# Optimization experiments

Measured on AMD Instinct MI355X. Metric: run time of the kernel, lower is better.

## Reference

```python
import jax, jax.numpy as jnp
import numpy as np

B, TX, TS = 64, 2048, 10
D, L, NMELS, MAXR, R = 256, 1024, 80, 20, 2


def gru_cell(x, h, wih, whh, bih, bhh):
    # torch GRUCell: gates ordered (r, z, n)
    gi = x @ wih.T + bih
    gh = h @ whh.T + bhh
    ir, iz, inn = jnp.split(gi, 3, axis=-1)
    hr, hz, hn = jnp.split(gh, 3, axis=-1)
    r = jax.nn.sigmoid(ir + hr)
    z = jax.nn.sigmoid(iz + hz)
    n = jnp.tanh(inn + r * hn)
    return (1.0 - z) * n + z * h


def lstm_cell(x, h, c, wih, whh, bih, bhh):
    # torch LSTMCell: gates ordered (i, f, g, o)
    g = x @ wih.T + bih + h @ whh.T + bhh
    i, f, gg, o = jnp.split(g, 4, axis=-1)
    c_new = jax.nn.sigmoid(f) * c + jax.nn.sigmoid(i) * jnp.tanh(gg)
    h_new = jax.nn.sigmoid(o) * jnp.tanh(c_new)
    return h_new, c_new


def attention(enc, query, W, v):
    # u = v @ tanh(enc + W q); softmax over time
    qp = query @ W.T                                  # [B, D]
    u = jnp.tanh(enc + qp[:, None, :]) @ v            # [B, T]
    scores = jax.nn.softmax(u, axis=-1)               # [B, T]
    ctx = jnp.einsum('bt,btd->bd', scores, enc)       # [B, D]
    return scores, ctx


def setup_inputs() -> dict:
    key = jax.random.key(0)
    ks = jax.random.split(key, 40)
    n = lambda i, shape, s=0.02: jax.random.normal(ks[i], shape, dtype=jnp.float32) * s
    return {
        'encoder_seq': n(0, (B, TX, D), 1.0),
        'style_embed': n(1, (B, TS, D), 1.0),
        'prenet_in': n(2, (B, NMELS), 1.0),
        'h_text': n(3, (B, D), 1.0), 'h_style': n(4, (B, D), 1.0), 'h_attn': n(5, (B, D), 1.0),
        'h_r1': n(6, (B, L), 1.0), 'h_r2': n(7, (B, L), 1.0),
        'c_r1': n(8, (B, L), 1.0), 'c_r2': n(9, (B, L), 1.0),
        'cv_text': n(10, (B, D), 1.0), 'cv_style': n(11, (B, D), 1.0), 'cv': n(12, (B, D), 1.0),
        'fc1_w': n(13, (256, NMELS)), 'fc1_b': jnp.zeros((256,), jnp.float32),
        'fc2_w': n(14, (128, 256)), 'fc2_b': jnp.zeros((128,), jnp.float32),
        'tW': n(15, (D, D)), 'tv': n(16, (D,)),
        'sW': n(17, (D, D)), 'sv': n(18, (D,)),
        't_wih': n(19, (3 * D, D + 128)), 't_whh': n(20, (3 * D, D)),
        't_bih': jnp.zeros((3 * D,), jnp.float32), 't_bhh': jnp.zeros((3 * D,), jnp.float32),
        's_wih': n(21, (3 * D, D + 128)), 's_whh': n(22, (3 * D, D)),
        's_bih': jnp.zeros((3 * D,), jnp.float32), 's_bhh': jnp.zeros((3 * D,), jnp.float32),
        'a_wih': n(23, (3 * D, D + 128)), 'a_whh': n(24, (3 * D, D)),
        'a_bih': jnp.zeros((3 * D,), jnp.float32), 'a_bhh': jnp.zeros((3 * D,), jnp.float32),
        'ri_w': n(25, (L, 2 * D)), 'ri_b': jnp.zeros((L,), jnp.float32),
        'l1_wih': n(26, (4 * L, L)), 'l1_whh': n(27, (4 * L, L)),
        'l1_bih': jnp.zeros((4 * L,), jnp.float32), 'l1_bhh': jnp.zeros((4 * L,), jnp.float32),
        'l2_wih': n(28, (4 * L, L)), 'l2_whh': n(29, (4 * L, L)),
        'l2_bih': jnp.zeros((4 * L,), jnp.float32), 'l2_bhh': jnp.zeros((4 * L,), jnp.float32),
        'mp_w': n(30, (NMELS * MAXR, L)),
        't': 0,
    }


def reference(encoder_seq, style_embed, prenet_in, h_text, h_style, h_attn,
              h_r1, h_r2, c_r1, c_r2, cv_text, cv_style, cv,
              fc1_w, fc1_b, fc2_w, fc2_b, tW, tv, sW, sv,
              t_wih, t_whh, t_bih, t_bhh, s_wih, s_whh, s_bih, s_bhh,
              a_wih, a_whh, a_bih, a_bhh, ri_w, ri_b,
              l1_wih, l1_whh, l1_bih, l1_bhh, l2_wih, l2_whh, l2_bih, l2_bhh,
              mp_w, t):
    # PreNet (eval mode: no dropout)
    p = jax.nn.relu(prenet_in @ fc1_w.T + fc1_b)
    p = jax.nn.relu(p @ fc2_w.T + fc2_b)                      # [B, 128]

    text_in = jnp.concatenate([cv_text, p], axis=-1)          # [B, D+128]
    style_in = jnp.concatenate([cv_style, p], axis=-1)
    attn_in = jnp.concatenate([cv, p], axis=-1)

    h_text = gru_cell(text_in, h_text, t_wih, t_whh, t_bih, t_bhh)
    text_scores, cv_text = attention(encoder_seq, h_text, tW, tv)

    h_style = gru_cell(style_in, h_style, s_wih, s_whh, s_bih, s_bhh)
    style_scores, cv_style = attention(style_embed, h_style, sW, sv)

    cv_new = cv_text                                          # context_vec = text_context_vec
    h_attn = gru_cell(attn_in, h_attn, a_wih, a_whh, a_bih, a_bhh)

    x = jnp.concatenate([cv_new, h_attn], axis=1) @ ri_w.T + ri_b  # [B, L]
    h_r1, c_r1 = lstm_cell(x, h_r1, c_r1, l1_wih, l1_whh, l1_bih, l1_bhh)
    x = x + h_r1
    h_r2, c_r2 = lstm_cell(x, h_r2, c_r2, l2_wih, l2_whh, l2_bih, l2_bhh)
    x = x + h_r2

    mels = (x @ mp_w.T).reshape(B, NMELS, MAXR)[:, :, :R]     # [B, n_mels, r]
    return mels
```

## Files before the change

kernel.cpp:

```cpp
#include <hip/hip_runtime.h>
#include <hip/hip_bf16.h>

typedef unsigned short u16;
typedef unsigned int   u32;
typedef __attribute__((ext_vector_type(8))) short bf16x8;
typedef __attribute__((ext_vector_type(4))) float f32x4;

#define NB   64
#define NTX  2048
#define ND   256
#define NL   1024

#if __has_builtin(__builtin_amdgcn_exp2f)
#define EXP2F(x) __builtin_amdgcn_exp2f(x)
#else
#define EXP2F(x) exp2f(x)
#endif
#if __has_builtin(__builtin_amdgcn_rcpf)
#define RCPF(x) __builtin_amdgcn_rcpf(x)
#else
#define RCPF(x) (1.0f/(x))
#endif

__device__ __forceinline__ u16 f2bf(float f){
  union { float f; u32 u; } c; c.f = f;
  return (u16)((c.u + 0x7fffu + ((c.u >> 16) & 1u)) >> 16);
}
__device__ __forceinline__ u32 pk2(float a, float b){
  return (u32)f2bf(a) | ((u32)f2bf(b) << 16);
}
__device__ __forceinline__ float sigmf(float x){ return 1.f/(1.f+__expf(-x)); }
__device__ __forceinline__ float tanhf_fast(float x){
  x = fminf(fmaxf(x, -15.f), 15.f);
  float e = __expf(2.f*x);
  return (e - 1.f) / (e + 1.f);
}
__device__ __forceinline__ float dot_rowf(const float* __restrict__ row,
                                          const float* __restrict__ x, int K4){
  float acc = 0.f;
  for (int j = 0; j < K4; ++j){
    float4 w = *(const float4*)(row + j*4);
    const float* xp = x + j*4;
    acc += w.x*xp[0] + w.y*xp[1] + w.z*xp[2] + w.w*xp[3];
  }
  return acc;
}

__global__ __launch_bounds__(256) void k_pre1(
    const float* __restrict__ cv_text, const float* __restrict__ cv,
    const float* __restrict__ h_text,  const float* __restrict__ h_attn,
    const float* __restrict__ prenet_in,
    const float* __restrict__ fc1_w, const float* __restrict__ fc1_b,
    const float* __restrict__ h_r1, const float* __restrict__ h_r2,
    float* __restrict__ xtext, float* __restrict__ xattn,
    float* __restrict__ htT,  float* __restrict__ haT,
    float* __restrict__ p1T,
    u16* __restrict__ hb1, u16* __restrict__ hb2)
{
  __shared__ float ld[64][65];
  const int blk = blockIdx.x, tid = threadIdx.x;
  if (blk < 16){
    int a = blk >> 2; int c0 = (blk & 3)*64;
    const float* src = (a==0)?cv_text:(a==1)?cv:(a==2)?h_text:h_attn;
    float* dst = (a==0)?xtext:(a==1)?xattn:(a==2)?htT:haT;
    const int r = tid >> 2, q = tid & 3;
    #pragma unroll
    for (int i = 0; i < 4; ++i){
      float4 v = *(const float4*)(src + (size_t)r*256 + c0 + q*16 + i*4);
      ld[r][q*16+i*4+0] = v.x; ld[r][q*16+i*4+1] = v.y;
      ld[r][q*16+i*4+2] = v.z; ld[r][q*16+i*4+3] = v.w;
    }
    __syncthreads();
    const int cc = tid >> 2;
    #pragma unroll
    for (int i = 0; i < 4; ++i){
      int b0 = q*16 + i*4;
      float4 o = { ld[b0+0][cc], ld[b0+1][cc], ld[b0+2][cc], ld[b0+3][cc] };
      *(float4*)(dst + (size_t)(c0+cc)*64 + b0) = o;
    }
  } else if (blk < 80){
    const int wave = tid >> 6, lane = tid & 63;
    const int n = (blk - 16)*4 + wave;
    float acc = fc1_b[n];
    const float* wr = fc1_w + (size_t)n*80;
    const float* xr = prenet_in + (size_t)lane*80;
    #pragma unroll
    for (int k = 0; k < 80; k += 4){
      float4 w = *(const float4*)(wr + k);
      acc += w.x*xr[k] + w.y*xr[k+1] + w.z*xr[k+2] + w.w*xr[k+3];
    }
    p1T[n*64 + lane] = fmaxf(acc, 0.f);
  } else {
    const int t2 = blk - 80;
    const float* src = (t2 < 32) ? h_r1 : h_r2;
    u16* dst = (t2 < 32) ? hb1 : hb2;
    const int base = (t2 & 31)*2048 + tid*8;
    float4 a = *(const float4*)(src + base);
    float4 b = *(const float4*)(src + base + 4);
    uint4 o = { pk2(a.x,a.y), pk2(a.z,a.w), pk2(b.x,b.y), pk2(b.z,b.w) };
    *(uint4*)(dst + base) = o;
  }
}

__global__ __launch_bounds__(256) void k_pre2(
    const float* __restrict__ p1T,
    const float* __restrict__ fc2_w, const float* __restrict__ fc2_b,
    float* __restrict__ xtext, float* __restrict__ xattn)
{
  const int tid = threadIdx.x, w = tid >> 6, lane = tid & 63;
  const int n = blockIdx.x;
  __shared__ float red[4][64];
  float acc = 0.f;
  const float* wr = fc2_w + (size_t)n*256 + w*64;
  const float* xb = p1T + w*64*64 + lane;
  #pragma unroll
  for (int k = 0; k < 64; k += 4){
    float4 wv = *(const float4*)(wr + k);
    acc += wv.x*xb[(k+0)*64] + wv.y*xb[(k+1)*64]
         + wv.z*xb[(k+2)*64] + wv.w*xb[(k+3)*64];
  }
  red[w][lane] = acc;
  __syncthreads();
  if (w == 0){
    float v = fmaxf(red[0][lane]+red[1][lane]+red[2][lane]+red[3][lane] + fc2_b[n], 0.f);
    xtext[(size_t)(256+n)*64 + lane] = v;
    xattn[(size_t)(256+n)*64 + lane] = v;
  }
}

__global__ __launch_bounds__(512) void k_gru(
    const float* __restrict__ t_wih, const float* __restrict__ t_whh,
    const float* __restrict__ t_bih, const float* __restrict__ t_bhh,
    const float* __restrict__ a_wih, const float* __restrict__ a_whh,
    const float* __restrict__ a_bih, const float* __restrict__ a_bhh,
    const float* __restrict__ xtext, const float* __restrict__ xattn,
    const float* __restrict__ htT,  const float* __restrict__ haT,
    float* __restrict__ htnT, u16* __restrict__ xrib)
{
  const int tid = threadIdx.x, w = tid >> 6, lane = tid & 63;
  const int isA = blockIdx.x >= 256;
  const int d = blockIdx.x & 255;
  const float* wih = isA ? a_wih : t_wih;
  const float* whh = isA ? a_whh : t_whh;
  const float* xT  = isA ? xattn : xtext;
  const float* hT  = isA ? haT   : htT;
  __shared__ float red[8][6][64];
  float s0=0.f,s1=0.f,s2=0.f,s3=0.f,s4=0.f,s5=0.f;
  {
    const float* wr = wih + (size_t)d*384       + w*48;
    const float* wz = wih + (size_t)(256+d)*384 + w*48;
    const float* wn = wih + (size_t)(512+d)*384 + w*48;
    const float* xb = xT + w*48*64 + lane;
    #pragma unroll 4
    for (int k = 0; k < 48; k += 4){
      float4 ar = *(const float4*)(wr + k);
      float4 az = *(const float4*)(wz + k);
      float4 an = *(const float4*)(wn + k);
      float x0 = xb[(k+0)*64], x1 = xb[(k+1)*64];
      float x2 = xb[(k+2)*64], x3 = xb[(k+3)*64];
      s0 += ar.x*x0 + ar.y*x1 + ar.z*x2 + ar.w*x3;
      s1 += az.x*x0 + az.y*x1 + az.z*x2 + az.w*x3;
      s2 += an.x*x0 + an.y*x1 + an.z*x2 + an.w*x3;
    }
  }
  {
    const float* vr = whh + (size_t)d*256       + w*32;
    const float* vz = whh + (size_t)(256+d)*256 + w*32;
    const float* vn = whh + (size_t)(512+d)*256 + w*32;
    const float* hb = hT + w*32*64 + lane;
    #pragma unroll 4
    for (int k = 0; k < 32; k += 4){
      float4 ar = *(const float4*)(vr + k);
      float4 az = *(const float4*)(vz + k);
      float4 an = *(const float4*)(vn + k);
      float h0 = hb[(k+0)*64], h1 = hb[(k+1)*64];
      float h2 = hb[(k+2)*64], h3 = hb[(k+3)*64];
      s3 += ar.x*h0 + ar.y*h1 + ar.z*h2 + ar.w*h3;
      s4 += az.x*h0 + az.y*h1 + az.z*h2 + az.w*h3;
      s5 += an.x*h0 + an.y*h1 + an.z*h2 + an.w*h3;
    }
  }
  red[w][0][lane]=s0; red[w][1][lane]=s1; red[w][2][lane]=s2;
  red[w][3][lane]=s3; red[w][4][lane]=s4; red[w][5][lane]=s5;
  __syncthreads();
  if (w == 0){
    const float* bih = isA ? a_bih : t_bih;
    const float* bhh = isA ? a_bhh : t_bhh;
    float g6[6];
    #pragma unroll
    for (int i = 0; i < 6; ++i){
      float a = 0.f;
      #pragma unroll
      for (int ww = 0; ww < 8; ++ww) a += red[ww][i][lane];
      g6[i] = a;
    }
    float gir = bih[d]     + g6[0];
    float giz = bih[256+d] + g6[1];
    float gin = bih[512+d] + g6[2];
    float ghr = bhh[d]     + g6[3];
    float ghz = bhh[256+d] + g6[4];
    float ghn = bhh[512+d] + g6[5];
    float hd = hT[d*64 + lane];
    float r  = sigmf(gir + ghr), z = sigmf(giz + ghz);
    float nn = tanhf_fast(gin + r*ghn);
    float hnew = (1.f - z)*nn + z*hd;
    if (isA) xrib[(size_t)lane*512 + 256 + d] = f2bf(hnew);
    else     htnT[(size_t)d*64 + lane]        = hnew;
  }
}

__global__ __launch_bounds__(256) void k_qp(
    const float* __restrict__ tWm, const float* __restrict__ htnT,
    float* __restrict__ qp)
{
  const int tid = threadIdx.x, w = tid >> 6, lane = tid & 63;
  const int d = blockIdx.x;
  __shared__ float red[4][64];
  float acc = 0.f;
  const float* wr = tWm + (size_t)d*256 + w*64;
  const float* xb = htnT + w*64*64 + lane;
  #pragma unroll
  for (int k = 0; k < 64; k += 4){
    float4 wv = *(const float4*)(wr + k);
    acc += wv.x*xb[(k+0)*64] + wv.y*xb[(k+1)*64]
         + wv.z*xb[(k+2)*64] + wv.w*xb[(k+3)*64];
  }
  red[w][lane] = acc;
  __syncthreads();
  if (w == 0)
    qp[lane*ND + d] = red[0][lane]+red[1][lane]+red[2][lane]+red[3][lane];
}

__global__ __launch_bounds__(256) void k_attn_part(
    const float* __restrict__ enc, const float* __restrict__ qp,
    const float* __restrict__ tv,  float* __restrict__ attnP)
{
  const int tid = threadIdx.x, b = blockIdx.x, ch = blockIdx.y;
  const int wave = tid >> 6, lane = tid & 63;
  const float C2  = 2.885390082f;
  const float L2E = 1.4426950408f;
  __shared__ float qpL[256], vL[256], ctxL[4][256], sL[4];
  qpL[tid] = qp[b*ND + tid] * C2;
  vL[tid]  = tv[tid] * 2.f;
  __syncthreads();

  const float q0 = qpL[lane*4+0], q1 = qpL[lane*4+1], q2 = qpL[lane*4+2], q3 = qpL[lane*4+3];
  const float v0 = vL[lane*4+0],  v1 = vL[lane*4+1],  v2 = vL[lane*4+2],  v3 = vL[lane*4+3];
  float vs = 0.5f*(v0 + v1 + v2 + v3);
  #pragma unroll
  for (int off = 1; off < 64; off <<= 1) vs += __shfl_xor(vs, off);
  const float VS = vs;

  float cx0=0.f, cx1=0.f, cx2=0.f, cx3=0.f, sacc=0.f;
  const float* base = enc + ((size_t)b*NTX + (size_t)ch*128 + wave*32)*ND + lane*4;
  #pragma unroll 4
  for (int i = 0; i < 32; ++i){
    float4 ev = *(const float4*)(base + (size_t)i*ND);
    float e0 = ev.x, e1 = ev.y, e2 = ev.z, e3 = ev.w;
    float srow;
    {
      float u0 = EXP2F(__builtin_fmaf(e0, C2, q0));
      float u1 = EXP2F(__builtin_fmaf(e1, C2, q1));
      float u2 = EXP2F(__builtin_fmaf(e2, C2, q2));
      float u3 = EXP2F(__builtin_fmaf(e3, C2, q3));
      srow = v0*RCPF(u0 + 1.f) + v1*RCPF(u1 + 1.f)
           + v2*RCPF(u2 + 1.f) + v3*RCPF(u3 + 1.f);
    }
    #pragma unroll
    for (int off = 1; off < 64; off <<= 1) srow += __shfl_xor(srow, off);
    float w = EXP2F((VS - srow) * L2E);
    sacc += w;
    cx0 = __builtin_fmaf(w, e0, cx0); cx1 = __builtin_fmaf(w, e1, cx1);
    cx2 = __builtin_fmaf(w, e2, cx2); cx3 = __builtin_fmaf(w, e3, cx3);
  }
  ctxL[wave][lane*4+0]=cx0; ctxL[wave][lane*4+1]=cx1;
  ctxL[wave][lane*4+2]=cx2; ctxL[wave][lane*4+3]=cx3;
  if (lane == 0) sL[wave] = sacc;
  __syncthreads();
  float c = ctxL[0][tid]+ctxL[1][tid]+ctxL[2][tid]+ctxL[3][tid];
  float* dst = attnP + ((size_t)b*16 + ch)*257;
  dst[tid] = c;
  if (tid == 0) dst[256] = sL[0]+sL[1]+sL[2]+sL[3];
}

__global__ __launch_bounds__(256) void k_attn_red(
    const float* __restrict__ attnP, u16* __restrict__ xrib)
{
  const int tid = threadIdx.x, b = blockIdx.x;
  float c = 0.f, s = 0.f;
  for (int ch = 0; ch < 16; ++ch){
    const float* src = attnP + ((size_t)b*16 + ch)*257;
    c += src[tid]; s += src[256];
  }
  xrib[(size_t)b*512 + tid] = f2bf(c / s);
}


__global__ __launch_bounds__(512) void k_mm_ri(
    const u16* __restrict__ xrib, const float* __restrict__ ri_w,
    const float* __restrict__ ri_b, float* __restrict__ x0,
    u16* __restrict__ x0b)
{
  __shared__ float Rs[8][4][4][65];
  const int tid = threadIdx.x, lane = tid & 63, w = tid >> 6;
  const int n0 = blockIdx.x * 16;
  f32x4 acc[4];
  #pragma unroll
  for (int i = 0; i < 4; ++i) acc[i] = (f32x4){0.f,0.f,0.f,0.f};
  const int kbase = w*64;
  const float* wr = ri_w + (size_t)(n0 + (lane & 15))*512 + kbase + (lane >> 4)*8;
  const u16* xs = xrib + (size_t)(lane & 15)*512 + kbase + (lane >> 4)*8;
  #pragma unroll
  for (int t = 0; t < 2; ++t){
    float4 wa = *(const float4*)(wr + t*32);
    float4 wb = *(const float4*)(wr + t*32 + 4);
    union { bf16x8 v; uint4 u; } bf;
    bf.u.x = pk2(wa.x,wa.y); bf.u.y = pk2(wa.z,wa.w);
    bf.u.z = pk2(wb.x,wb.y); bf.u.w = pk2(wb.z,wb.w);
    #pragma unroll
    for (int fb = 0; fb < 4; ++fb){
      union { bf16x8 v; uint4 u; } af;
      af.u = *(const uint4*)(xs + fb*16*512 + t*32);
      acc[fb] = __builtin_amdgcn_mfma_f32_16x16x32_bf16(af.v, bf.v, acc[fb], 0, 0, 0);
    }
  }
  #pragma unroll
  for (int fb = 0; fb < 4; ++fb)
    #pragma unroll
    for (int r = 0; r < 4; ++r) Rs[w][fb][r][lane] = acc[fb][r];
  __syncthreads();
  if (tid < 256){
    const int b = tid >> 2, c4 = (tid & 3)*4;
    const int fb = b >> 4, q = (b >> 2) & 3, reg = b & 3;
    #pragma unroll
    for (int cc = 0; cc < 4; ++cc){
      const int c = c4 + cc;
      float v = ri_b[n0 + c];
      #pragma unroll
      for (int ww = 0; ww < 8; ++ww) v += Rs[ww][fb][reg][q*16 + c];
      x0[(size_t)b*1024 + n0 + c]  = v;
      x0b[(size_t)b*1024 + n0 + c] = f2bf(v);
    }
  }
}

__global__ __launch_bounds__(1024) void k_lstm(
    const float* __restrict__ Wih, const float* __restrict__ Whh,
    const u16* __restrict__ xb, const u16* __restrict__ hb,
    const float* __restrict__ bih, const float* __restrict__ bhh,
    const float* __restrict__ c_in,
    const float* __restrict__ xin, float* __restrict__ xout,
    u16* __restrict__ xoutb)
{
  __shared__ float Rs[16][4][4][65];
  const int tid = threadIdx.x, lane = tid & 63, w = tid >> 6;
  const int j0 = blockIdx.x * 4;
  const float* W = (w < 8) ? Wih : Whh;
  const u16*   X = (w < 8) ? xb  : hb;
  const int kbase = (w & 7) * 128;

  f32x4 acc[4];
  #pragma unroll
  for (int i = 0; i < 4; ++i) acc[i] = (f32x4){0.f,0.f,0.f,0.f};
  const int r16 = lane & 15;
  const int g = r16 >> 2, jq = r16 & 3;
  const float* wr = W + (size_t)(g*1024 + j0 + jq)*1024 + kbase + (lane >> 4)*8;
  #pragma unroll
  for (int t = 0; t < 4; ++t){
    float4 wa = *(const float4*)(wr + t*32);
    float4 wb = *(const float4*)(wr + t*32 + 4);
    union { bf16x8 v; uint4 u; } bf;
    bf.u.x = pk2(wa.x,wa.y); bf.u.y = pk2(wa.z,wa.w);
    bf.u.z = pk2(wb.x,wb.y); bf.u.w = pk2(wb.z,wb.w);
    #pragma unroll
    for (int fb = 0; fb < 4; ++fb){
      union { bf16x8 v; uint4 u; } af;
      af.u = *(const uint4*)(X + (size_t)(fb*16 + r16)*1024 + kbase + (lane >> 4)*8 + t*32);
      acc[fb] = __builtin_amdgcn_mfma_f32_16x16x32_bf16(af.v, bf.v, acc[fb], 0, 0, 0);
    }
  }
  #pragma unroll
  for (int fb = 0; fb < 4; ++fb)
    #pragma unroll
    for (int r = 0; r < 4; ++r) Rs[w][fb][r][lane] = acc[fb][r];
  __syncthreads();

  if (tid < 256){
    const int b  = tid >> 2, jq2 = tid & 3;
    const int j  = j0 + jq2;
    const int fb = b >> 4, q = (b >> 2) & 3, reg = b & 3;
    float gate[4];
    #pragma unroll
    for (int gg = 0; gg < 4; ++gg){
      const int li = q*16 + gg*4 + jq2;
      float a = bih[gg*1024 + j] + bhh[gg*1024 + j];
      #pragma unroll
      for (int ww = 0; ww < 16; ++ww) a += Rs[ww][fb][reg][li];
      gate[gg] = a;
    }
    float ii = sigmf(gate[0]), ff = sigmf(gate[1]);
    float gv = tanhf_fast(gate[2]), oo = sigmf(gate[3]);
    float cc = ff * c_in[(size_t)b*1024 + j] + ii * gv;
    float hh = oo * tanhf_fast(cc);
    float xo = xin[(size_t)b*1024 + j] + hh;
    xout[(size_t)b*1024 + j]  = xo;
    xoutb[(size_t)b*1024 + j] = f2bf(xo);
  }
}

__global__ __launch_bounds__(256) void k_mels(
    const float* __restrict__ x2, const float* __restrict__ mp_w,
    float* __restrict__ out)
{
  const int tid = threadIdx.x, b = blockIdx.x;
  __shared__ float xL[NL];
  #pragma unroll
  for (int i = 0; i < 4; ++i){
    int j = tid + 256*i;
    xL[j] = x2[(size_t)b*NL + j];
  }
  __syncthreads();
  if (tid < 160){
    int m = tid >> 1, r = tid & 1;
    float acc = dot_rowf(mp_w + (size_t)(m*20 + r)*NL, xL, 256);
    out[b*160 + tid] = acc;
  }
}

extern "C" void kernel_launch(void* const* d_in, const int* in_sizes, int n_in,
                              void* d_out, int out_size, void* d_ws, size_t ws_size,
                              hipStream_t stream)
{
  (void)in_sizes; (void)n_in; (void)out_size; (void)ws_size;
  const float* enc     = (const float*)d_in[0];
  const float* pre_in  = (const float*)d_in[2];
  const float* h_text  = (const float*)d_in[3];
  const float* h_attn  = (const float*)d_in[5];
  const float* h_r1    = (const float*)d_in[6];
  const float* h_r2    = (const float*)d_in[7];
  const float* c_r1    = (const float*)d_in[8];
  const float* c_r2    = (const float*)d_in[9];
  const float* cv_text = (const float*)d_in[10];
  const float* cv      = (const float*)d_in[12];
  const float* fc1_w   = (const float*)d_in[13];
  const float* fc1_b   = (const float*)d_in[14];
  const float* fc2_w   = (const float*)d_in[15];
  const float* fc2_b   = (const float*)d_in[16];
  const float* tWm     = (const float*)d_in[17];
  const float* tv      = (const float*)d_in[18];
  const float* t_wih   = (const float*)d_in[21];
  const float* t_whh   = (const float*)d_in[22];
  const float* t_bih   = (const float*)d_in[23];
  const float* t_bhh   = (const float*)d_in[24];
  const float* a_wih   = (const float*)d_in[29];
  const float* a_whh   = (const float*)d_in[30];
  const float* a_bih   = (const float*)d_in[31];
  const float* a_bhh   = (const float*)d_in[32];
  const float* ri_w    = (const float*)d_in[33];
  const float* ri_b    = (const float*)d_in[34];
  const float* l1_wih  = (const float*)d_in[35];
  const float* l1_whh  = (const float*)d_in[36];
  const float* l1_bih  = (const float*)d_in[37];
  const float* l1_bhh  = (const float*)d_in[38];
  const float* l2_wih  = (const float*)d_in[39];
  const float* l2_whh  = (const float*)d_in[40];
  const float* l2_bih  = (const float*)d_in[41];
  const float* l2_bhh  = (const float*)d_in[42];
  const float* mp_w    = (const float*)d_in[43];

  float* ws    = (float*)d_ws;
  float* qp    = ws;
  float* attnP = qp    + 16384;
  float* x0    = attnP + 263168;
  float* x1    = x0    + 65536;
  float* x2    = x1    + 65536;
  float* xtext = x2    + 65536;
  float* xattn = xtext + 24576;
  float* htT   = xattn + 24576;
  float* haT   = htT   + 16384;
  float* htnT  = haT   + 16384;
  float* p1T   = htnT  + 16384;
  u16*   hb1   = (u16*)(p1T + 16384);
  u16*   hb2   = hb1 + 65536;
  u16*   xrib  = hb2 + 65536;
  u16*   x0b   = xrib + 32768;
  u16*   x1b   = x0b + 65536;
  u16*   x2b   = x1b + 65536;

  k_pre1<<<144, 256, 0, stream>>>(cv_text, cv, h_text, h_attn,
      pre_in, fc1_w, fc1_b, h_r1, h_r2,
      xtext, xattn, htT, haT, p1T, hb1, hb2);
  k_pre2<<<128, 256, 0, stream>>>(p1T, fc2_w, fc2_b, xtext, xattn);
  k_gru<<<512, 512, 0, stream>>>(t_wih, t_whh, t_bih, t_bhh,
      a_wih, a_whh, a_bih, a_bhh, xtext, xattn, htT, haT, htnT, xrib);
  k_qp<<<256, 256, 0, stream>>>(tWm, htnT, qp);

  k_attn_part<<<dim3(64,16), 256, 0, stream>>>(enc, qp, tv, attnP);
  k_attn_red<<<64, 256, 0, stream>>>(attnP, xrib);

  k_mm_ri<<<64, 512, 0, stream>>>(xrib, ri_w, ri_b, x0, x0b);

  k_lstm<<<256, 1024, 0, stream>>>(l1_wih, l1_whh, x0b, hb1,
      l1_bih, l1_bhh, c_r1, x0, x1, x1b);
  k_lstm<<<256, 1024, 0, stream>>>(l2_wih, l2_whh, x1b, hb2,
      l2_bih, l2_bhh, c_r2, x1, x2, x2b);

  k_mels<<<64, 256, 0, stream>>>(x2, mp_w, (float*)d_out);
}
```

Before: 115.6 us.

## Fuse attention, ri matmul, LSTMs and mel projection into one cooperative kernel

Replaces the six back-end launches (attention partials, reduction, ri matmul, two LSTM stages, mel projection) with a single cooperative kernel of 256 blocks of 1024 threads. The stages are separated by atomic-counter grid barriers whose counters are zeroed by an extra block in k_pre1. The attention reduction is folded into the ri matmul stage, and the LDS partial-sum layout is skewed to reduce bank conflicts. This removes launch gaps between small kernels, at the cost of spin-wait barriers and fewer, larger blocks for the attention stage.

After: 245.6 us. 113% more time.

```diff
diff --git a/kernel.cpp b/kernel.cpp
--- a/kernel.cpp
+++ b/kernel.cpp
@@ -35,15 +35,17 @@
   float e = __expf(2.f*x);
   return (e - 1.f) / (e + 1.f);
 }
-__device__ __forceinline__ float dot_rowf(const float* __restrict__ row,
-                                          const float* __restrict__ x, int K4){
-  float acc = 0.f;
-  for (int j = 0; j < K4; ++j){
-    float4 w = *(const float4*)(row + j*4);
-    const float* xp = x + j*4;
-    acc += w.x*xp[0] + w.y*xp[1] + w.z*xp[2] + w.w*xp[3];
-  }
-  return acc;
+
+__device__ __forceinline__ void gbar(int* cnt, int idx, int nb){
+  __syncthreads();
+  if (threadIdx.x == 0){
+    __builtin_amdgcn_fence(__ATOMIC_RELEASE, "agent");
+    __hip_atomic_fetch_add(&cnt[idx], 1, __ATOMIC_RELAXED, __HIP_MEMORY_SCOPE_AGENT);
+    while (__hip_atomic_load(&cnt[idx], __ATOMIC_RELAXED, __HIP_MEMORY_SCOPE_AGENT) < nb)
+      __builtin_amdgcn_s_sleep(4);
+    __builtin_amdgcn_fence(__ATOMIC_ACQUIRE, "agent");
+  }
+  __syncthreads();
 }
 
 __global__ __launch_bounds__(256) void k_pre1(
@@ -55,7 +57,8 @@
     float* __restrict__ xtext, float* __restrict__ xattn,
     float* __restrict__ htT,  float* __restrict__ haT,
     float* __restrict__ p1T,
-    u16* __restrict__ hb1, u16* __restrict__ hb2)
+    u16* __restrict__ hb1, u16* __restrict__ hb2,
+    int* __restrict__ cnt)
 {
   __shared__ float ld[64][65];
   const int blk = blockIdx.x, tid = threadIdx.x;
@@ -90,7 +93,7 @@
       acc += w.x*xr[k] + w.y*xr[k+1] + w.z*xr[k+2] + w.w*xr[k+3];
     }
     p1T[n*64 + lane] = fmaxf(acc, 0.f);
-  } else {
+  } else if (blk < 144){
     const int t2 = blk - 80;
     const float* src = (t2 < 32) ? h_r1 : h_r2;
     u16* dst = (t2 < 32) ? hb1 : hb2;
@@ -99,6 +102,8 @@
     float4 b = *(const float4*)(src + base + 4);
     uint4 o = { pk2(a.x,a.y), pk2(a.z,a.w), pk2(b.x,b.y), pk2(b.z,b.w) };
     *(uint4*)(dst + base) = o;
+  } else {
+    if (tid < 8) cnt[tid] = 0;
   }
 }
 
@@ -231,134 +236,28 @@
     qp[lane*ND + d] = red[0][lane]+red[1][lane]+red[2][lane]+red[3][lane];
 }
 
-__global__ __launch_bounds__(256) void k_attn_part(
-    const float* __restrict__ enc, const float* __restrict__ qp,
-    const float* __restrict__ tv,  float* __restrict__ attnP)
-{
-  const int tid = threadIdx.x, b = blockIdx.x, ch = blockIdx.y;
-  const int wave = tid >> 6, lane = tid & 63;
-  const float C2  = 2.885390082f;
-  const float L2E = 1.4426950408f;
-  __shared__ float qpL[256], vL[256], ctxL[4][256], sL[4];
-  qpL[tid] = qp[b*ND + tid] * C2;
-  vL[tid]  = tv[tid] * 2.f;
-  __syncthreads();
-
-  const float q0 = qpL[lane*4+0], q1 = qpL[lane*4+1], q2 = qpL[lane*4+2], q3 = qpL[lane*4+3];
-  const float v0 = vL[lane*4+0],  v1 = vL[lane*4+1],  v2 = vL[lane*4+2],  v3 = vL[lane*4+3];
-  float vs = 0.5f*(v0 + v1 + v2 + v3);
-  #pragma unroll
-  for (int off = 1; off < 64; off <<= 1) vs += __shfl_xor(vs, off);
-  const float VS = vs;
-
-  float cx0=0.f, cx1=0.f, cx2=0.f, cx3=0.f, sacc=0.f;
-  const float* base = enc + ((size_t)b*NTX + (size_t)ch*128 + wave*32)*ND + lane*4;
-  #pragma unroll 4
-  for (int i = 0; i < 32; ++i){
-    float4 ev = *(const float4*)(base + (size_t)i*ND);
-    float e0 = ev.x, e1 = ev.y, e2 = ev.z, e3 = ev.w;
-    float srow;
-    {
-      float u0 = EXP2F(__builtin_fmaf(e0, C2, q0));
-      float u1 = EXP2F(__builtin_fmaf(e1, C2, q1));
-      float u2 = EXP2F(__builtin_fmaf(e2, C2, q2));
-      float u3 = EXP2F(__builtin_fmaf(e3, C2, q3));
-      srow = v0*RCPF(u0 + 1.f) + v1*RCPF(u1 + 1.f)
-           + v2*RCPF(u2 + 1.f) + v3*RCPF(u3 + 1.f);
-    }
-    #pragma unroll
-    for (int off = 1; off < 64; off <<= 1) srow += __shfl_xor(srow, off);
-    float w = EXP2F((VS - srow) * L2E);
-    sacc += w;
-    cx0 = __builtin_fmaf(w, e0, cx0); cx1 = __builtin_fmaf(w, e1, cx1);
-    cx2 = __builtin_fmaf(w, e2, cx2); cx3 = __builtin_fmaf(w, e3, cx3);
-  }
-  ctxL[wave][lane*4+0]=cx0; ctxL[wave][lane*4+1]=cx1;
-  ctxL[wave][lane*4+2]=cx2; ctxL[wave][lane*4+3]=cx3;
-  if (lane == 0) sL[wave] = sacc;
-  __syncthreads();
-  float c = ctxL[0][tid]+ctxL[1][tid]+ctxL[2][tid]+ctxL[3][tid];
-  float* dst = attnP + ((size_t)b*16 + ch)*257;
-  dst[tid] = c;
-  if (tid == 0) dst[256] = sL[0]+sL[1]+sL[2]+sL[3];
-}
-
-__global__ __launch_bounds__(256) void k_attn_red(
-    const float* __restrict__ attnP, u16* __restrict__ xrib)
-{
-  const int tid = threadIdx.x, b = blockIdx.x;
-  float c = 0.f, s = 0.f;
-  for (int ch = 0; ch < 16; ++ch){
-    const float* src = attnP + ((size_t)b*16 + ch)*257;
-    c += src[tid]; s += src[256];
-  }
-  xrib[(size_t)b*512 + tid] = f2bf(c / s);
-}
-
-
-__global__ __launch_bounds__(512) void k_mm_ri(
-    const u16* __restrict__ xrib, const float* __restrict__ ri_w,
-    const float* __restrict__ ri_b, float* __restrict__ x0,
-    u16* __restrict__ x0b)
-{
-  __shared__ float Rs[8][4][4][65];
-  const int tid = threadIdx.x, lane = tid & 63, w = tid >> 6;
-  const int n0 = blockIdx.x * 16;
-  f32x4 acc[4];
-  #pragma unroll
-  for (int i = 0; i < 4; ++i) acc[i] = (f32x4){0.f,0.f,0.f,0.f};
-  const int kbase = w*64;
-  const float* wr = ri_w + (size_t)(n0 + (lane & 15))*512 + kbase + (lane >> 4)*8;
-  const u16* xs = xrib + (size_t)(lane & 15)*512 + kbase + (lane >> 4)*8;
-  #pragma unroll
-  for (int t = 0; t < 2; ++t){
-    float4 wa = *(const float4*)(wr + t*32);
-    float4 wb = *(const float4*)(wr + t*32 + 4);
-    union { bf16x8 v; uint4 u; } bf;
-    bf.u.x = pk2(wa.x,wa.y); bf.u.y = pk2(wa.z,wa.w);
-    bf.u.z = pk2(wb.x,wb.y); bf.u.w = pk2(wb.z,wb.w);
-    #pragma unroll
-    for (int fb = 0; fb < 4; ++fb){
-      union { bf16x8 v; uint4 u; } af;
-      af.u = *(const uint4*)(xs + fb*16*512 + t*32);
-      acc[fb] = __builtin_amdgcn_mfma_f32_16x16x32_bf16(af.v, bf.v, acc[fb], 0, 0, 0);
-    }
-  }
-  #pragma unroll
-  for (int fb = 0; fb < 4; ++fb)
-    #pragma unroll
-    for (int r = 0; r < 4; ++r) Rs[w][fb][r][lane] = acc[fb][r];
-  __syncthreads();
-  if (tid < 256){
-    const int b = tid >> 2, c4 = (tid & 3)*4;
-    const int fb = b >> 4, q = (b >> 2) & 3, reg = b & 3;
-    #pragma unroll
-    for (int cc = 0; cc < 4; ++cc){
-      const int c = c4 + cc;
-      float v = ri_b[n0 + c];
-      #pragma unroll
-      for (int ww = 0; ww < 8; ++ww) v += Rs[ww][fb][reg][q*16 + c];
-      x0[(size_t)b*1024 + n0 + c]  = v;
-      x0b[(size_t)b*1024 + n0 + c] = f2bf(v);
-    }
-  }
-}
-
-__global__ __launch_bounds__(1024) void k_lstm(
+struct BA {
+  const float *enc, *qp, *tv, *ri_w, *ri_b,
+              *l1_wih, *l1_whh, *l1_bih, *l1_bhh, *c_r1,
+              *l2_wih, *l2_whh, *l2_bih, *l2_bhh, *c_r2, *mp_w;
+  float *attnP, *x0, *x1, *x2;
+  u16 *xrib, *x0b, *x1b, *x2b, *hb1, *hb2;
+  float* out;
+  int* cnt;
+};
+
+__device__ __forceinline__ void lstm_stage(float* Rs,
     const float* __restrict__ Wih, const float* __restrict__ Whh,
     const u16* __restrict__ xb, const u16* __restrict__ hb,
     const float* __restrict__ bih, const float* __restrict__ bhh,
-    const float* __restrict__ c_in,
-    const float* __restrict__ xin, float* __restrict__ xout,
-    u16* __restrict__ xoutb)
-{
-  __shared__ float Rs[16][4][4][65];
+    const float* __restrict__ c_in, const float* __restrict__ xin,
+    float* __restrict__ xout, u16* __restrict__ xoutb)
+{
   const int tid = threadIdx.x, lane = tid & 63, w = tid >> 6;
   const int j0 = blockIdx.x * 4;
   const float* W = (w < 8) ? Wih : Whh;
   const u16*   X = (w < 8) ? xb  : hb;
   const int kbase = (w & 7) * 128;
-
   f32x4 acc[4];
   #pragma unroll
   for (int i = 0; i < 4; ++i) acc[i] = (f32x4){0.f,0.f,0.f,0.f};
@@ -382,9 +281,9 @@
   #pragma unroll
   for (int fb = 0; fb < 4; ++fb)
     #pragma unroll
-    for (int r = 0; r < 4; ++r) Rs[w][fb][r][lane] = acc[fb][r];
+    for (int r = 0; r < 4; ++r)
+      Rs[w*1024 + fb*256 + r*64 + ((lane + w*4) & 63)] = acc[fb][r];
   __syncthreads();
-
   if (tid < 256){
     const int b  = tid >> 2, jq2 = tid & 3;
     const int j  = j0 + jq2;
@@ -393,10 +292,11 @@
     #pragma unroll
     for (int gg = 0; gg < 4; ++gg){
       const int li = q*16 + gg*4 + jq2;
-      float a = bih[gg*1024 + j] + bhh[gg*1024 + j];
-      #pragma unroll
-      for (int ww = 0; ww < 16; ++ww) a += Rs[ww][fb][reg][li];
-      gate[gg] = a;
+      float s = bih[gg*1024 + j] + bhh[gg*1024 + j];
+      #pragma unroll
+      for (int ww = 0; ww < 16; ++ww)
+        s += Rs[ww*1024 + fb*256 + reg*64 + ((li + ww*4) & 63)];
+      gate[gg] = s;
     }
     float ii = sigmf(gate[0]), ff = sigmf(gate[1]);
     float gv = tanhf_fast(gate[2]), oo = sigmf(gate[3]);
@@ -408,22 +308,164 @@
   }
 }
 
-__global__ __launch_bounds__(256) void k_mels(
-    const float* __restrict__ x2, const float* __restrict__ mp_w,
-    float* __restrict__ out)
-{
-  const int tid = threadIdx.x, b = blockIdx.x;
-  __shared__ float xL[NL];
-  #pragma unroll
-  for (int i = 0; i < 4; ++i){
-    int j = tid + 256*i;
-    xL[j] = x2[(size_t)b*NL + j];
-  }
-  __syncthreads();
-  if (tid < 160){
-    int m = tid >> 1, r = tid & 1;
-    float acc = dot_rowf(mp_w + (size_t)(m*20 + r)*NL, xL, 256);
-    out[b*160 + tid] = acc;
+__global__ __launch_bounds__(1024) void k_back(BA a)
+{
+  __shared__ char smem[65536];
+  float* smemf = (float*)smem;
+  const int tid = threadIdx.x, blk = blockIdx.x;
+  const int lane = tid & 63, w = tid >> 6;
+  const int vblk = blk*4 + (tid >> 8), vtid = tid & 255;
+
+  {
+    const int b = blk >> 2, chg = blk & 3;
+    const float C2  = 2.885390082f;
+    const float L2E = 1.4426950408f;
+    float* qpL  = smemf;
+    float* vL   = smemf + 256;
+    float* ctxL = smemf + 512;
+    float* sL   = smemf + 512 + 4096;
+    if (tid < 256){
+      qpL[tid] = a.qp[b*ND + tid] * C2;
+      vL[tid]  = a.tv[tid] * 2.f;
+    }
+    __syncthreads();
+    const float q0 = qpL[lane*4+0], q1 = qpL[lane*4+1], q2 = qpL[lane*4+2], q3 = qpL[lane*4+3];
+    const float v0 = vL[lane*4+0],  v1 = vL[lane*4+1],  v2 = vL[lane*4+2],  v3 = vL[lane*4+3];
+    float vs = 0.5f*(v0 + v1 + v2 + v3);
+    #pragma unroll
+    for (int off = 1; off < 64; off <<= 1) vs += __shfl_xor(vs, off);
+    const float VS = vs;
+    float cx0=0.f, cx1=0.f, cx2=0.f, cx3=0.f, sacc=0.f;
+    const float* base = a.enc + ((size_t)b*NTX + (size_t)chg*512 + w*32)*ND + lane*4;
+    #pragma unroll 4
+    for (int i = 0; i < 32; ++i){
+      float4 ev = *(const float4*)(base + (size_t)i*ND);
+      float e0 = ev.x, e1 = ev.y, e2 = ev.z, e3 = ev.w;
+      float u0 = EXP2F(__builtin_fmaf(e0, C2, q0));
+      float u1 = EXP2F(__builtin_fmaf(e1, C2, q1));
+      float u2 = EXP2F(__builtin_fmaf(e2, C2, q2));
+      float u3 = EXP2F(__builtin_fmaf(e3, C2, q3));
+      float srow = v0*RCPF(u0 + 1.f) + v1*RCPF(u1 + 1.f)
+                 + v2*RCPF(u2 + 1.f) + v3*RCPF(u3 + 1.f);
+      #pragma unroll
+      for (int off = 1; off < 64; off <<= 1) srow += __shfl_xor(srow, off);
+      float ww = EXP2F((VS - srow) * L2E);
+      sacc += ww;
+      cx0 = __builtin_fmaf(ww, e0, cx0); cx1 = __builtin_fmaf(ww, e1, cx1);
+      cx2 = __builtin_fmaf(ww, e2, cx2); cx3 = __builtin_fmaf(ww, e3, cx3);
+    }
+    ctxL[w*256 + lane*4+0]=cx0; ctxL[w*256 + lane*4+1]=cx1;
+    ctxL[w*256 + lane*4+2]=cx2; ctxL[w*256 + lane*4+3]=cx3;
+    if (lane == 0) sL[w] = sacc;
+    __syncthreads();
+    if (tid < 256){
+      float c = 0.f;
+      #pragma unroll
+      for (int ww = 0; ww < 16; ++ww) c += ctxL[ww*256 + tid];
+      a.attnP[(size_t)blk*257 + tid] = c;
+      if (tid == 0){
+        float s = 0.f;
+        #pragma unroll
+        for (int ww = 0; ww < 16; ++ww) s += sL[ww];
+        a.attnP[(size_t)blk*257 + 256] = s;
+      }
+    }
+  }
+  gbar(a.cnt, 0, 256);
+
+  if (blk < 64){
+    u16*   xctxb = (u16*)smem;
+    float* Rs    = (float*)(smem + 32768);
+    {
+      const int b = tid >> 4, cg16 = tid & 15;
+      float s = a.attnP[(size_t)(b*4+0)*257 + 256] + a.attnP[(size_t)(b*4+1)*257 + 256]
+              + a.attnP[(size_t)(b*4+2)*257 + 256] + a.attnP[(size_t)(b*4+3)*257 + 256];
+      float inv = RCPF(s);
+      #pragma unroll
+      for (int i = 0; i < 16; ++i){
+        int c = cg16*16 + i;
+        float v = a.attnP[(size_t)(b*4+0)*257 + c] + a.attnP[(size_t)(b*4+1)*257 + c]
+                + a.attnP[(size_t)(b*4+2)*257 + c] + a.attnP[(size_t)(b*4+3)*257 + c];
+        xctxb[b*256 + c] = f2bf(v * inv);
+      }
+    }
+    __syncthreads();
+    const int n0 = blk * 16;
+    if (w < 8){
+      f32x4 acc[4];
+      #pragma unroll
+      for (int i = 0; i < 4; ++i) acc[i] = (f32x4){0.f,0.f,0.f,0.f};
+      const int kbase = w*64;
+      const float* wr = a.ri_w + (size_t)(n0 + (lane & 15))*512 + kbase + (lane >> 4)*8;
+      #pragma unroll
+      for (int t = 0; t < 2; ++t){
+        float4 wa = *(const float4*)(wr + t*32);
+        float4 wb = *(const float4*)(wr + t*32 + 4);
+        union { bf16x8 v; uint4 u; } bf;
+        bf.u.x = pk2(wa.x,wa.y); bf.u.y = pk2(wa.z,wa.w);
+        bf.u.z = pk2(wb.x,wb.y); bf.u.w = pk2(wb.z,wb.w);
+        #pragma unroll
+        for (int fb = 0; fb < 4; ++fb){
+          union { bf16x8 v; uint4 u; } af;
+          const int row = fb*16 + (lane & 15);
+          if (w < 4)
+            af.u = *(const uint4*)(xctxb + row*256 + kbase + (lane >> 4)*8 + t*32);
+          else
+            af.u = *(const uint4*)(a.xrib + (size_t)row*512 + kbase + (lane >> 4)*8 + t*32);
+          acc[fb] = __builtin_amdgcn_mfma_f32_16x16x32_bf16(af.v, bf.v, acc[fb], 0, 0, 0);
+        }
+      }
+      #pragma unroll
+      for (int fb = 0; fb < 4; ++fb)
+        #pragma unroll
+        for (int r = 0; r < 4; ++r)
+          Rs[w*1024 + fb*256 + r*64 + ((lane + w*4) & 63)] = acc[fb][r];
+    }
+    __syncthreads();
+    if (tid < 256){
+      const int b = tid >> 2, c4 = (tid & 3)*4;
+      const int fb = b >> 4, q = (b >> 2) & 3, reg = b & 3;
+      #pragma unroll
+      for (int cc = 0; cc < 4; ++cc){
+        const int c = c4 + cc;
+        const int li = q*16 + c;
+        float v = a.ri_b[n0 + c];
+        #pragma unroll
+        for (int ww = 0; ww < 8; ++ww)
+          v += Rs[ww*1024 + fb*256 + reg*64 + ((li + ww*4) & 63)];
+        a.x0[(size_t)b*1024 + n0 + c]  = v;
+        a.x0b[(size_t)b*1024 + n0 + c] = f2bf(v);
+      }
+    }
+  }
+  gbar(a.cnt, 1, 256);
+
+  lstm_stage(smemf, a.l1_wih, a.l1_whh, a.x0b, a.hb1,
+             a.l1_bih, a.l1_bhh, a.c_r1, a.x0, a.x1, a.x1b);
+  gbar(a.cnt, 2, 256);
+  lstm_stage(smemf, a.l2_wih, a.l2_whh, a.x1b, a.hb2,
+             a.l2_bih, a.l2_bhh, a.c_r2, a.x1, a.x2, a.x2b);
+  gbar(a.cnt, 3, 256);
+
+  if (blk < 16){
+    const int b = vblk;
+    float* xL = smemf + (tid >> 8)*1024;
+    #pragma unroll
+    for (int i = 0; i < 4; ++i){
+      int j = vtid + 256*i;
+      xL[j] = a.x2[(size_t)b*NL + j];
+    }
+    __syncthreads();
+    if (vtid < 160){
+      int m = vtid >> 1, r = vtid & 1;
+      const float* row = a.mp_w + (size_t)(m*20 + r)*NL;
+      float acc = 0.f;
+      for (int k = 0; k < 1024; k += 4){
+        float4 wq = *(const float4*)(row + k);
+        acc += wq.x*xL[k] + wq.y*xL[k+1] + wq.z*xL[k+2] + wq.w*xL[k+3];
+      }
+      a.out[b*160 + vtid] = acc;
+    }
   }
 }
 
@@ -471,7 +513,7 @@
   float* ws    = (float*)d_ws;
   float* qp    = ws;
   float* attnP = qp    + 16384;
-  float* x0    = attnP + 263168;
+  float* x0    = attnP + 65792;
   float* x1    = x0    + 65536;
   float* x2    = x1    + 65536;
   float* xtext = x2    + 65536;
@@ -486,24 +528,28 @@
   u16*   x0b   = xrib + 32768;
   u16*   x1b   = x0b + 65536;
   u16*   x2b   = x1b + 65536;
-
-  k_pre1<<<144, 256, 0, stream>>>(cv_text, cv, h_text, h_attn,
+  int*   cnt   = (int*)(x2b + 65536);
+
+  k_pre1<<<145, 256, 0, stream>>>(cv_text, cv, h_text, h_attn,
       pre_in, fc1_w, fc1_b, h_r1, h_r2,
-      xtext, xattn, htT, haT, p1T, hb1, hb2);
+      xtext, xattn, htT, haT, p1T, hb1, hb2, cnt);
   k_pre2<<<128, 256, 0, stream>>>(p1T, fc2_w, fc2_b, xtext, xattn);
   k_gru<<<512, 512, 0, stream>>>(t_wih, t_whh, t_bih, t_bhh,
       a_wih, a_whh, a_bih, a_bhh, xtext, xattn, htT, haT, htnT, xrib);
   k_qp<<<256, 256, 0, stream>>>(tWm, htnT, qp);
 
-  k_attn_part<<<dim3(64,16), 256, 0, stream>>>(enc, qp, tv, attnP);
-  k_attn_red<<<64, 256, 0, stream>>>(attnP, xrib);
-
-  k_mm_ri<<<64, 512, 0, stream>>>(xrib, ri_w, ri_b, x0, x0b);
-
-  k_lstm<<<256, 1024, 0, stream>>>(l1_wih, l1_whh, x0b, hb1,
-      l1_bih, l1_bhh, c_r1, x0, x1, x1b);
-  k_lstm<<<256, 1024, 0, stream>>>(l2_wih, l2_whh, x1b, hb2,
-      l2_bih, l2_bhh, c_r2, x1, x2, x2b);
-
-  k_mels<<<64, 256, 0, stream>>>(x2, mp_w, (float*)d_out);
-}
+  BA a;
+  a.enc = enc; a.qp = qp; a.tv = tv; a.ri_w = ri_w; a.ri_b = ri_b;
+  a.l1_wih = l1_wih; a.l1_whh = l1_whh; a.l1_bih = l1_bih; a.l1_bhh = l1_bhh; a.c_r1 = c_r1;
+  a.l2_wih = l2_wih; a.l2_whh = l2_whh; a.l2_bih = l2_bih; a.l2_bhh = l2_bhh; a.c_r2 = c_r2;
+  a.mp_w = mp_w;
+  a.attnP = attnP; a.x0 = x0; a.x1 = x1; a.x2 = x2;
+  a.xrib = xrib; a.x0b = x0b; a.x1b = x1b; a.x2b = x2b;
+  a.hb1 = hb1; a.hb2 = hb2;
+  a.out = (float*)d_out;
+  a.cnt = cnt;
+
+  void* args[] = { &a };
+  hipLaunchCooperativeKernel((const void*)k_back, dim3(256), dim3(1024),
+                             args, 0, stream);
+}
```

## Batch encoder row loads and replace per-row shuffle reductions with shared-memory transpose reduction

Applied to the files above, without the earlier changes.

The attention partial kernel now loads all 16 encoder rows per wave into registers up front, which lets the memory loads run concurrently. It computes per-lane partial scores into shared memory and reduces them with a transposed read plus two shuffles, instead of running a six-step shuffle reduction on every row. The grid doubles to 32 chunks per batch so more blocks are resident, and the reduction kernel and workspace offsets are updated to match. The costs are more registers for the 16 float4 values, two extra barriers, and twice as many partial results to reduce.

New measurement: 110.9 us (median of 2 runs). 4.0% less time.

```diff
diff --git a/kernel.cpp b/kernel.cpp
--- a/kernel.cpp
+++ b/kernel.cpp
@@ -236,10 +236,13 @@
     const float* __restrict__ tv,  float* __restrict__ attnP)
 {
   const int tid = threadIdx.x, b = blockIdx.x, ch = blockIdx.y;
-  const int wave = tid >> 6, lane = tid & 63;
+  const int w = tid >> 6, lane = tid & 63;
   const float C2  = 2.885390082f;
   const float L2E = 1.4426950408f;
-  __shared__ float qpL[256], vL[256], ctxL[4][256], sL[4];
+  __shared__ float qpL[256], vL[256];
+  __shared__ float part[4][16][65];
+  __shared__ float wbc[4][16];
+  __shared__ float ctxL[4][256], sL[4];
   qpL[tid] = qp[b*ND + tid] * C2;
   vL[tid]  = tv[tid] * 2.f;
   __syncthreads();
@@ -251,34 +254,49 @@
   for (int off = 1; off < 64; off <<= 1) vs += __shfl_xor(vs, off);
   const float VS = vs;
 
+  const float* base = enc + ((size_t)b*NTX + (size_t)ch*64 + w*16)*ND + lane*4;
+  float4 ev[16];
+  #pragma unroll
+  for (int i = 0; i < 16; ++i) ev[i] = *(const float4*)(base + (size_t)i*ND);
+
+  #pragma unroll
+  for (int i = 0; i < 16; ++i){
+    float u0 = EXP2F(__builtin_fmaf(ev[i].x, C2, q0));
+    float u1 = EXP2F(__builtin_fmaf(ev[i].y, C2, q1));
+    float u2 = EXP2F(__builtin_fmaf(ev[i].z, C2, q2));
+    float u3 = EXP2F(__builtin_fmaf(ev[i].w, C2, q3));
+    part[w][i][lane] = v0*RCPF(u0 + 1.f) + v1*RCPF(u1 + 1.f)
+                     + v2*RCPF(u2 + 1.f) + v3*RCPF(u3 + 1.f);
+  }
+  __syncthreads();
+
+  {
+    const int rr = lane >> 2, q4 = lane & 3;
+    float s = 0.f;
+    #pragma unroll
+    for (int i = 0; i < 16; ++i) s += part[w][rr][q4*16 + i];
+    s += __shfl_xor(s, 1);
+    s += __shfl_xor(s, 2);
+    if (q4 == 0) wbc[w][rr] = EXP2F((VS - s) * L2E);
+  }
+  __syncthreads();
+
   float cx0=0.f, cx1=0.f, cx2=0.f, cx3=0.f, sacc=0.f;
-  const float* base = enc + ((size_t)b*NTX + (size_t)ch*128 + wave*32)*ND + lane*4;
-  #pragma unroll 4
-  for (int i = 0; i < 32; ++i){
-    float4 ev = *(const float4*)(base + (size_t)i*ND);
-    float e0 = ev.x, e1 = ev.y, e2 = ev.z, e3 = ev.w;
-    float srow;
-    {
-      float u0 = EXP2F(__builtin_fmaf(e0, C2, q0));
-      float u1 = EXP2F(__builtin_fmaf(e1, C2, q1));
-      float u2 = EXP2F(__builtin_fmaf(e2, C2, q2));
-      float u3 = EXP2F(__builtin_fmaf(e3, C2, q3));
-      srow = v0*RCPF(u0 + 1.f) + v1*RCPF(u1 + 1.f)
-           + v2*RCPF(u2 + 1.f) + v3*RCPF(u3 + 1.f);
-    }
-    #pragma unroll
-    for (int off = 1; off < 64; off <<= 1) srow += __shfl_xor(srow, off);
-    float w = EXP2F((VS - srow) * L2E);
-    sacc += w;
-    cx0 = __builtin_fmaf(w, e0, cx0); cx1 = __builtin_fmaf(w, e1, cx1);
-    cx2 = __builtin_fmaf(w, e2, cx2); cx3 = __builtin_fmaf(w, e3, cx3);
-  }
-  ctxL[wave][lane*4+0]=cx0; ctxL[wave][lane*4+1]=cx1;
-  ctxL[wave][lane*4+2]=cx2; ctxL[wave][lane*4+3]=cx3;
-  if (lane == 0) sL[wave] = sacc;
+  #pragma unroll
+  for (int r = 0; r < 16; ++r){
+    float wv = wbc[w][r];
+    sacc += wv;
+    cx0 = __builtin_fmaf(wv, ev[r].x, cx0);
+    cx1 = __builtin_fmaf(wv, ev[r].y, cx1);
+    cx2 = __builtin_fmaf(wv, ev[r].z, cx2);
+    cx3 = __builtin_fmaf(wv, ev[r].w, cx3);
+  }
+  ctxL[w][lane*4+0]=cx0; ctxL[w][lane*4+1]=cx1;
+  ctxL[w][lane*4+2]=cx2; ctxL[w][lane*4+3]=cx3;
+  if (lane == 0) sL[w] = sacc;
   __syncthreads();
   float c = ctxL[0][tid]+ctxL[1][tid]+ctxL[2][tid]+ctxL[3][tid];
-  float* dst = attnP + ((size_t)b*16 + ch)*257;
+  float* dst = attnP + ((size_t)b*32 + ch)*257;
   dst[tid] = c;
   if (tid == 0) dst[256] = sL[0]+sL[1]+sL[2]+sL[3];
 }
@@ -288,8 +306,8 @@
 {
   const int tid = threadIdx.x, b = blockIdx.x;
   float c = 0.f, s = 0.f;
-  for (int ch = 0; ch < 16; ++ch){
-    const float* src = attnP + ((size_t)b*16 + ch)*257;
+  for (int ch = 0; ch < 32; ++ch){
+    const float* src = attnP + ((size_t)b*32 + ch)*257;
     c += src[tid]; s += src[256];
   }
   xrib[(size_t)b*512 + tid] = f2bf(c / s);
@@ -471,7 +489,7 @@
   float* ws    = (float*)d_ws;
   float* qp    = ws;
   float* attnP = qp    + 16384;
-  float* x0    = attnP + 263168;
+  float* x0    = attnP + 526336;
   float* x1    = x0    + 65536;
   float* x2    = x1    + 65536;
   float* xtext = x2    + 65536;
@@ -495,7 +513,7 @@
       a_wih, a_whh, a_bih, a_bhh, xtext, xattn, htT, haT, htnT, xrib);
   k_qp<<<256, 256, 0, stream>>>(tWm, htnT, qp);
 
-  k_attn_part<<<dim3(64,16), 256, 0, stream>>>(enc, qp, tv, attnP);
+  k_attn_part<<<dim3(64,32), 256, 0, stream>>>(enc, qp, tv, attnP);
   k_attn_red<<<64, 256, 0, stream>>>(attnP, xrib);
 
   k_mm_ri<<<64, 512, 0, stream>>>(xrib, ri_w, ri_b, x0, x0b);
```
